# Optimization experiments

Measured on AMD Instinct MI355X. Metric: run time of the kernel, lower is better.

Reference implementation:

```python
import jax, jax.numpy as jnp
import numpy as np

NUM_PARTS = 10
COP_W = 10.0
COP_K = 100.0
RES = 0.7874


def setup_inputs() -> dict:
    key = jax.random.key(0)
    k1, k2, k3, k4, k5, k6 = jax.random.split(key, 6)
    B, V, F, NHD = 256, 6890, 13776, 20000
    vertices = jax.random.normal(k1, (B, V, 3), dtype=jnp.float32)
    pressure = jax.random.uniform(k2, (B, 120, 40), dtype=jnp.float32)
    bw = jax.random.uniform(k3, (NHD, 3), dtype=jnp.float32)
    bary_w = bw / bw.sum(axis=1, keepdims=True)  # barycentric weights sum to 1
    faces = jax.random.randint(k4, (F, 3), 0, V, dtype=jnp.int64)
    face_sample = jax.random.randint(k5, (NHD,), 0, F, dtype=jnp.int64)
    face_part = jax.random.randint(k6, (F,), 0, NUM_PARTS, dtype=jnp.int64)
    return {"vertices": vertices, "pressure": pressure, "bary_w": bary_w,
            "faces": faces, "face_sample": face_sample, "face_part": face_part}


def cal_cop(pressure, resolution=RES):
    B, Y, X = pressure.shape
    x_coords = jnp.arange(X, dtype=pressure.dtype)
    y_coords = jnp.arange(Y, dtype=pressure.dtype)
    total = pressure.sum(axis=(1, 2))
    total = jnp.where(total == 0, jnp.asarray(1e-8, pressure.dtype), total)
    x_ws = (pressure * x_coords).sum(axis=(1, 2))
    y_ws = (pressure * y_coords[:, None]).sum(axis=(1, 2))
    x_c = x_ws / total
    y_c = y_ws / total
    cop_x = 0.01 * (x_c - 18.0) / resolution
    cop_y = 0.01 * (86.0 - y_c) / resolution
    cop_xy = jnp.stack([cop_x, cop_y, jnp.zeros_like(cop_x)], axis=1)
    cop_sensor_xy = jnp.stack([x_c, y_c], axis=1)
    return cop_xy, cop_sensor_xy


def reference(vertices, pressure, bary_w, faces, face_sample, face_part):
    # ---- per-part volume: signed tetrahedron volume per face, segment-summed per part
    tri = vertices[:, faces]                       # [B, F, 3, 3]
    v0, v1, v2 = tri[:, :, 0], tri[:, :, 1], tri[:, :, 2]
    tet = jnp.einsum('bfi,bfi->bf', v0, jnp.cross(v1, v2)) / 6.0   # [B, F]
    per_part_volume = jax.vmap(
        lambda t: jax.ops.segment_sum(t, face_part, num_segments=NUM_PARTS)
    )(tet)                                          # [B, P]

    # ---- HD mesh: barycentric sampling of 20000 points from faces
    fv = faces[face_sample]                         # [NHD, 3]
    vertices_hd = jnp.einsum('bnkc,nk->bnc', vertices[:, fv], bary_w)  # [B, NHD, 3]

    # ---- vertex-id -> part-volume mapping (one-hot sparse matmul == gather)
    vol_per_vert = per_part_volume[:, face_part[face_sample]]          # [B, NHD]

    com = (vertices_hd * vol_per_vert[..., None]).sum(axis=1) / \
          vol_per_vert.sum(axis=1, keepdims=True)                      # [B, 3]
    com_xy = jnp.stack([com[:, 0], com[:, 1], jnp.zeros_like(com[:, 0])], axis=1)
    com_mat = jnp.stack([com[:, 0] * 48.0, (59.0 / 33.0 - com[:, 1]) * 33.0], axis=1)

    cop_xy, _cop_mat = cal_cop(pressure)

    eps = 1e-6
    vh = vertices_hd[:, :, 1]                       # height above ground plane
    inside = (vh < 0.0).astype(vh.dtype)
    pw = inside * (1.0 - COP_K * vh) + (1.0 - inside) * jnp.exp(-COP_W * vh)
    cop = (vertices_hd * pw[..., None]).sum(axis=1) / (pw.sum(axis=1, keepdims=True) + eps)
    cop_mat_ipman = jnp.stack([cop[:, 0] + 18.0 / 78.74,
                               86.0 / 78.74 - cop[:, 1]], axis=1) * 100.0 * 0.7874

    stability_loss = jnp.linalg.norm(com_xy - cop_xy, axis=1).mean()
    return stability_loss, com_mat, cop_mat_ipman
```

## Files before the change

kernel.cpp:

```cpp
#include <hip/hip_runtime.h>
#include <math.h>

#define NB 256
#define NV 6890
#define NF 13776
#define NHD 20000
#define NPARTS 10
#define PY 120
#define PX 40
#define THREADS 1024
#define NWAVES (THREADS / 64)

#define WS_DIST_OFF  0
#define WS_TABF_OFF  1024
#define WS_TABS_OFF  (WS_TABF_OFF + NF * 16)
#define WS_TABW_OFF  (WS_TABS_OFF + NHD * 16)
#define WS_NEEDED    (WS_TABW_OFF + NHD * 16)

__device__ __forceinline__ float wred(float v) {
#pragma unroll
    for (int off = 32; off; off >>= 1) v += __shfl_down(v, off, 64);
    return v;
}

__global__ __launch_bounds__(256) void build_face_tab(const int* __restrict__ faces,
                                                      const int* __restrict__ face_part,
                                                      int4* __restrict__ tabF) {
    const int f = blockIdx.x * 256 + threadIdx.x;
    if (f < NF)
        tabF[f] = make_int4(faces[3 * f + 0], faces[3 * f + 1], faces[3 * f + 2], face_part[f]);
}

__global__ __launch_bounds__(256) void build_samp_tab(const int* __restrict__ faces,
                                                      const int* __restrict__ face_sample,
                                                      const int* __restrict__ face_part,
                                                      const float* __restrict__ bary_w,
                                                      int4* __restrict__ tabS,
                                                      float4* __restrict__ tabW) {
    const int n = blockIdx.x * 256 + threadIdx.x;
    if (n < NHD) {
        const int fs = face_sample[n];
        tabS[n] = make_int4(faces[3 * fs + 0], faces[3 * fs + 1], faces[3 * fs + 2], face_part[fs]);
        tabW[n] = make_float4(bary_w[3 * n + 0], bary_w[3 * n + 1], bary_w[3 * n + 2], 0.0f);
    }
}

template <bool TAB>
__global__ __launch_bounds__(THREADS, 4) void stab_main(
    const float* __restrict__ vertices,
    const float* __restrict__ pressure,
    const float* __restrict__ bary_w,
    const int*   __restrict__ faces,
    const int*   __restrict__ face_sample,
    const int*   __restrict__ face_part,
    const int4*  __restrict__ tabF,
    const int4*  __restrict__ tabS,
    const float4* __restrict__ tabW,
    float* __restrict__ out,
    float* __restrict__ dist)
{
    const int b    = blockIdx.x;
    const int tid  = threadIdx.x;
    const int wave = tid >> 6;
    const int lane = tid & 63;

    __shared__ float2 svxy[NV];
    __shared__ float  svz[NV];
    __shared__ float  red[NWAVES][12];
    __shared__ float  ppv[NPARTS];

    const float* vb = vertices + (size_t)b * (NV * 3);
    for (int v = tid; v < NV; v += THREADS) {
        const float x = vb[3 * v + 0];
        const float y = vb[3 * v + 1];
        const float z = vb[3 * v + 2];
        svxy[v] = make_float2(x, y);
        svz[v]  = z;
    }
    __syncthreads();

    float pv[NPARTS];
#pragma unroll
    for (int p = 0; p < NPARTS; ++p) pv[p] = 0.0f;

    for (int f = tid; f < NF; f += THREADS) {
        int i0, i1, i2, part;
        if constexpr (TAB) {
            const int4 q = tabF[f];
            i0 = q.x; i1 = q.y; i2 = q.z; part = q.w;
        } else {
            i0 = faces[3 * f + 0]; i1 = faces[3 * f + 1]; i2 = faces[3 * f + 2];
            part = face_part[f];
        }
        const float2 a = svxy[i0]; const float az = svz[i0];
        const float2 bb = svxy[i1]; const float bz = svz[i1];
        const float2 cc = svxy[i2]; const float cz = svz[i2];
        const float crx = bb.y * cz - bz * cc.y;
        const float cry = bz * cc.x - bb.x * cz;
        const float crz = bb.x * cc.y - bb.y * cc.x;
        const float tet = (a.x * crx + a.y * cry + az * crz) * (1.0f / 6.0f);
#pragma unroll
        for (int p = 0; p < NPARTS; ++p) pv[p] += (part == p) ? tet : 0.0f;
    }
#pragma unroll
    for (int p = 0; p < NPARTS; ++p) {
        const float r = wred(pv[p]);
        if (lane == 0) red[wave][p] = r;
    }
    __syncthreads();
    if (tid < NPARTS) {
        float s = 0.0f;
#pragma unroll
        for (int w = 0; w < NWAVES; ++w) s += red[w][tid];
        ppv[tid] = s;
    }
    __syncthreads();

    float cnx = 0.f, cny = 0.f, cd = 0.f;
    float pnx = 0.f, pny = 0.f, pd = 0.f;
    for (int n = tid; n < NHD; n += THREADS) {
        int i0, i1, i2, part;
        float w0, w1, w2;
        if constexpr (TAB) {
            const int4 q = tabS[n];
            const float4 w = tabW[n];
            i0 = q.x; i1 = q.y; i2 = q.z; part = q.w;
            w0 = w.x; w1 = w.y; w2 = w.z;
        } else {
            const int fs = face_sample[n];
            i0 = faces[3 * fs + 0]; i1 = faces[3 * fs + 1]; i2 = faces[3 * fs + 2];
            part = face_part[fs];
            w0 = bary_w[3 * n + 0]; w1 = bary_w[3 * n + 1]; w2 = bary_w[3 * n + 2];
        }
        const float2 p0 = svxy[i0];
        const float2 p1 = svxy[i1];
        const float2 p2 = svxy[i2];
        const float hx = w0 * p0.x + w1 * p1.x + w2 * p2.x;
        const float hy = w0 * p0.y + w1 * p1.y + w2 * p2.y;
        const float vol = ppv[part];
        cnx += hx * vol; cny += hy * vol; cd += vol;
        const float pw = (hy < 0.0f) ? (1.0f - 100.0f * hy) : __expf(-10.0f * hy);
        pnx += hx * pw; pny += hy * pw; pd += pw;
    }

    float pt = 0.f, pxs = 0.f, pys = 0.f;
    const float* pb = pressure + (size_t)b * (PY * PX);
    for (int i = tid; i < PY * PX; i += THREADS) {
        const float p  = pb[i];
        const float xi = (float)(i % PX);
        const float yi = (float)(i / PX);
        pt  += p;
        pxs += p * xi;
        pys += p * yi;
    }

    float vals[9] = {cnx, cny, cd, pnx, pny, pd, pt, pxs, pys};
#pragma unroll
    for (int k = 0; k < 9; ++k) {
        const float r = wred(vals[k]);
        if (lane == 0) red[wave][k] = r;
    }
    __syncthreads();

    if (tid == 0) {
        float s[9];
#pragma unroll
        for (int k = 0; k < 9; ++k) {
            float acc = 0.0f;
#pragma unroll
            for (int w = 0; w < NWAVES; ++w) acc += red[w][k];
            s[k] = acc;
        }
        const float comx  = s[0] / s[2];
        const float comy  = s[1] / s[2];
        const float copx  = s[3] / (s[5] + 1e-6f);
        const float copy_ = s[4] / (s[5] + 1e-6f);

        out[1 + 2 * b + 0] = comx * 48.0f;
        out[1 + 2 * b + 1] = (59.0f / 33.0f - comy) * 33.0f;
        out[1 + 2 * NB + 2 * b + 0] = (copx + 18.0f / 78.74f) * (100.0f * 0.7874f);
        out[1 + 2 * NB + 2 * b + 1] = (86.0f / 78.74f - copy_) * (100.0f * 0.7874f);

        const float total = (s[6] == 0.0f) ? 1e-8f : s[6];
        const float xc = s[7] / total;
        const float yc = s[8] / total;
        const float pcopx = 0.01f * (xc - 18.0f) / 0.7874f;
        const float pcopy = 0.01f * (86.0f - yc) / 0.7874f;

        const float dx = comx - pcopx;
        const float dy = comy - pcopy;
        dist[b] = sqrtf(dx * dx + dy * dy);
    }
}

__global__ __launch_bounds__(256) void stab_reduce(const float* __restrict__ dist,
                                                   float* __restrict__ out) {
    const int tid = threadIdx.x;
    float v = dist[tid];
    v = wred(v);
    __shared__ float red[4];
    if ((tid & 63) == 0) red[tid >> 6] = v;
    __syncthreads();
    if (tid == 0) out[0] = (red[0] + red[1] + red[2] + red[3]) * (1.0f / 256.0f);
}

extern "C" void kernel_launch(void* const* d_in, const int* in_sizes, int n_in,
                              void* d_out, int out_size, void* d_ws, size_t ws_size,
                              hipStream_t stream) {
    const float* vertices    = (const float*)d_in[0];
    const float* pressure    = (const float*)d_in[1];
    const float* bary_w      = (const float*)d_in[2];
    const int*   faces       = (const int*)d_in[3];
    const int*   face_sample = (const int*)d_in[4];
    const int*   face_part   = (const int*)d_in[5];
    float* out = (float*)d_out;
    char*  ws  = (char*)d_ws;

    float* dist = (float*)(ws + WS_DIST_OFF);

    if (ws_size >= (size_t)WS_NEEDED) {
        int4*   tabF = (int4*)(ws + WS_TABF_OFF);
        int4*   tabS = (int4*)(ws + WS_TABS_OFF);
        float4* tabW = (float4*)(ws + WS_TABW_OFF);
        build_face_tab<<<(NF + 255) / 256, 256, 0, stream>>>(faces, face_part, tabF);
        build_samp_tab<<<(NHD + 255) / 256, 256, 0, stream>>>(faces, face_sample, face_part,
                                                              bary_w, tabS, tabW);
        stab_main<true><<<NB, THREADS, 0, stream>>>(vertices, pressure, bary_w, faces,
                                                    face_sample, face_part, tabF, tabS, tabW,
                                                    out, dist);
    } else {
        stab_main<false><<<NB, THREADS, 0, stream>>>(vertices, pressure, bary_w, faces,
                                                     face_sample, face_part, nullptr, nullptr,
                                                     nullptr, out, dist);
    }
    stab_reduce<<<1, 256, 0, stream>>>(dist, out);
}
```

Before: 38.30 us.

## Merge table-build kernels, split vertex LDS into SoA, unroll gather loops by four

Merges the two index-table build kernels into one launch, which removes one kernel launch. Shared-memory vertex storage moves from float2+float to three separate float arrays. The face-volume and HD-sample loops in the table path are unrolled by four with clamped indices and masking, so more independent loads and LDS gathers are in flight per thread. The cost is higher register pressure at 1024 threads per block and extra LDS load instructions from the SoA split.

```diff
diff --git a/kernel.cpp b/kernel.cpp
--- a/kernel.cpp
+++ b/kernel.cpp
@@ -23,26 +23,31 @@
     return v;
 }
 
-__global__ __launch_bounds__(256) void build_face_tab(const int* __restrict__ faces,
-                                                      const int* __restrict__ face_part,
-                                                      int4* __restrict__ tabF) {
-    const int f = blockIdx.x * 256 + threadIdx.x;
-    if (f < NF)
-        tabF[f] = make_int4(faces[3 * f + 0], faces[3 * f + 1], faces[3 * f + 2], face_part[f]);
-}
-
-__global__ __launch_bounds__(256) void build_samp_tab(const int* __restrict__ faces,
-                                                      const int* __restrict__ face_sample,
-                                                      const int* __restrict__ face_part,
-                                                      const float* __restrict__ bary_w,
-                                                      int4* __restrict__ tabS,
-                                                      float4* __restrict__ tabW) {
-    const int n = blockIdx.x * 256 + threadIdx.x;
-    if (n < NHD) {
-        const int fs = face_sample[n];
-        tabS[n] = make_int4(faces[3 * fs + 0], faces[3 * fs + 1], faces[3 * fs + 2], face_part[fs]);
-        tabW[n] = make_float4(bary_w[3 * n + 0], bary_w[3 * n + 1], bary_w[3 * n + 2], 0.0f);
-    }
+__global__ __launch_bounds__(256) void build_tabs(const int* __restrict__ faces,
+                                                  const int* __restrict__ face_part,
+                                                  const int* __restrict__ face_sample,
+                                                  const float* __restrict__ bary_w,
+                                                  int4* __restrict__ tabF,
+                                                  int4* __restrict__ tabS,
+                                                  float4* __restrict__ tabW) {
+    const int i = blockIdx.x * 256 + threadIdx.x;
+    if (i < NF)
+        tabF[i] = make_int4(faces[3 * i + 0], faces[3 * i + 1], faces[3 * i + 2], face_part[i]);
+    if (i < NHD) {
+        const int fs = face_sample[i];
+        tabS[i] = make_int4(faces[3 * fs + 0], faces[3 * fs + 1], faces[3 * fs + 2], face_part[fs]);
+        tabW[i] = make_float4(bary_w[3 * i + 0], bary_w[3 * i + 1], bary_w[3 * i + 2], 0.0f);
+    }
+}
+
+__device__ __forceinline__ float tet_of(const float* __restrict__ svx,
+                                        const float* __restrict__ svy,
+                                        const float* __restrict__ svz, int4 q) {
+    const float ax = svx[q.x], bx = svx[q.y], cx = svx[q.z];
+    const float ay = svy[q.x], by = svy[q.y], cy = svy[q.z];
+    const float az = svz[q.x], bz = svz[q.y], cz = svz[q.z];
+    return (ax * (by * cz - bz * cy) + ay * (bz * cx - bx * cz) + az * (bx * cy - by * cx)) *
+           (1.0f / 6.0f);
 }
 
 template <bool TAB>
@@ -64,18 +69,17 @@
     const int wave = tid >> 6;
     const int lane = tid & 63;
 
-    __shared__ float2 svxy[NV];
-    __shared__ float  svz[NV];
-    __shared__ float  red[NWAVES][12];
-    __shared__ float  ppv[NPARTS];
+    __shared__ float svx[NV];
+    __shared__ float svy[NV];
+    __shared__ float svz[NV];
+    __shared__ float red[NWAVES][12];
+    __shared__ float ppv[NPARTS];
 
     const float* vb = vertices + (size_t)b * (NV * 3);
     for (int v = tid; v < NV; v += THREADS) {
-        const float x = vb[3 * v + 0];
-        const float y = vb[3 * v + 1];
-        const float z = vb[3 * v + 2];
-        svxy[v] = make_float2(x, y);
-        svz[v]  = z;
+        svx[v] = vb[3 * v + 0];
+        svy[v] = vb[3 * v + 1];
+        svz[v] = vb[3 * v + 2];
     }
     __syncthreads();
 
@@ -83,24 +87,37 @@
 #pragma unroll
     for (int p = 0; p < NPARTS; ++p) pv[p] = 0.0f;
 
-    for (int f = tid; f < NF; f += THREADS) {
-        int i0, i1, i2, part;
-        if constexpr (TAB) {
-            const int4 q = tabF[f];
-            i0 = q.x; i1 = q.y; i2 = q.z; part = q.w;
-        } else {
-            i0 = faces[3 * f + 0]; i1 = faces[3 * f + 1]; i2 = faces[3 * f + 2];
-            part = face_part[f];
-        }
-        const float2 a = svxy[i0]; const float az = svz[i0];
-        const float2 bb = svxy[i1]; const float bz = svz[i1];
-        const float2 cc = svxy[i2]; const float cz = svz[i2];
-        const float crx = bb.y * cz - bz * cc.y;
-        const float cry = bz * cc.x - bb.x * cz;
-        const float crz = bb.x * cc.y - bb.y * cc.x;
-        const float tet = (a.x * crx + a.y * cry + az * crz) * (1.0f / 6.0f);
-#pragma unroll
-        for (int p = 0; p < NPARTS; ++p) pv[p] += (part == p) ? tet : 0.0f;
+    if constexpr (TAB) {
+        for (int f0 = tid; f0 < NF; f0 += 4 * THREADS) {
+            const int f1 = f0 + THREADS, f2 = f0 + 2 * THREADS, f3 = f0 + 3 * THREADS;
+            const int g1 = min(f1, NF - 1), g2 = min(f2, NF - 1), g3 = min(f3, NF - 1);
+            const int4 q0 = tabF[f0];
+            const int4 q1 = tabF[g1];
+            const int4 q2 = tabF[g2];
+            const int4 q3 = tabF[g3];
+            const float m1 = (f1 < NF) ? 1.0f : 0.0f;
+            const float m2 = (f2 < NF) ? 1.0f : 0.0f;
+            const float m3 = (f3 < NF) ? 1.0f : 0.0f;
+            const float t0 = tet_of(svx, svy, svz, q0);
+            const float t1 = tet_of(svx, svy, svz, q1) * m1;
+            const float t2 = tet_of(svx, svy, svz, q2) * m2;
+            const float t3 = tet_of(svx, svy, svz, q3) * m3;
+#pragma unroll
+            for (int p = 0; p < NPARTS; ++p) {
+                pv[p] += (q0.w == p) ? t0 : 0.0f;
+                pv[p] += (q1.w == p) ? t1 : 0.0f;
+                pv[p] += (q2.w == p) ? t2 : 0.0f;
+                pv[p] += (q3.w == p) ? t3 : 0.0f;
+            }
+        }
+    } else {
+        for (int f = tid; f < NF; f += THREADS) {
+            const int4 q = make_int4(faces[3 * f + 0], faces[3 * f + 1], faces[3 * f + 2],
+                                     face_part[f]);
+            const float t = tet_of(svx, svy, svz, q);
+#pragma unroll
+            for (int p = 0; p < NPARTS; ++p) pv[p] += (q.w == p) ? t : 0.0f;
+        }
     }
 #pragma unroll
     for (int p = 0; p < NPARTS; ++p) {
@@ -118,29 +135,61 @@
 
     float cnx = 0.f, cny = 0.f, cd = 0.f;
     float pnx = 0.f, pny = 0.f, pd = 0.f;
-    for (int n = tid; n < NHD; n += THREADS) {
-        int i0, i1, i2, part;
-        float w0, w1, w2;
-        if constexpr (TAB) {
-            const int4 q = tabS[n];
-            const float4 w = tabW[n];
-            i0 = q.x; i1 = q.y; i2 = q.z; part = q.w;
-            w0 = w.x; w1 = w.y; w2 = w.z;
-        } else {
+
+    if constexpr (TAB) {
+        for (int n0 = tid; n0 < NHD; n0 += 4 * THREADS) {
+            const int n1 = n0 + THREADS, n2 = n0 + 2 * THREADS, n3 = n0 + 3 * THREADS;
+            const int h1 = min(n1, NHD - 1), h2 = min(n2, NHD - 1), h3 = min(n3, NHD - 1);
+            const int4 q0 = tabS[n0];
+            const int4 q1 = tabS[h1];
+            const int4 q2 = tabS[h2];
+            const int4 q3 = tabS[h3];
+            const float4 w0 = tabW[n0];
+            const float4 w1 = tabW[h1];
+            const float4 w2 = tabW[h2];
+            const float4 w3 = tabW[h3];
+            const float m1 = (n1 < NHD) ? 1.0f : 0.0f;
+            const float m2 = (n2 < NHD) ? 1.0f : 0.0f;
+            const float m3 = (n3 < NHD) ? 1.0f : 0.0f;
+
+            const float hx0 = w0.x * svx[q0.x] + w0.y * svx[q0.y] + w0.z * svx[q0.z];
+            const float hy0 = w0.x * svy[q0.x] + w0.y * svy[q0.y] + w0.z * svy[q0.z];
+            const float hx1 = w1.x * svx[q1.x] + w1.y * svx[q1.y] + w1.z * svx[q1.z];
+            const float hy1 = w1.x * svy[q1.x] + w1.y * svy[q1.y] + w1.z * svy[q1.z];
+            const float hx2 = w2.x * svx[q2.x] + w2.y * svx[q2.y] + w2.z * svx[q2.z];
+            const float hy2 = w2.x * svy[q2.x] + w2.y * svy[q2.y] + w2.z * svy[q2.z];
+            const float hx3 = w3.x * svx[q3.x] + w3.y * svx[q3.y] + w3.z * svx[q3.z];
+            const float hy3 = w3.x * svy[q3.x] + w3.y * svy[q3.y] + w3.z * svy[q3.z];
+
+            const float vol0 = ppv[q0.w];
+            const float vol1 = ppv[q1.w] * m1;
+            const float vol2 = ppv[q2.w] * m2;
+            const float vol3 = ppv[q3.w] * m3;
+
+            const float pw0 = ((hy0 < 0.0f) ? (1.0f - 100.0f * hy0) : __expf(-10.0f * hy0));
+            const float pw1 = ((hy1 < 0.0f) ? (1.0f - 100.0f * hy1) : __expf(-10.0f * hy1)) * m1;
+            const float pw2 = ((hy2 < 0.0f) ? (1.0f - 100.0f * hy2) : __expf(-10.0f * hy2)) * m2;
+            const float pw3 = ((hy3 < 0.0f) ? (1.0f - 100.0f * hy3) : __expf(-10.0f * hy3)) * m3;
+
+            cnx += hx0 * vol0 + hx1 * vol1 + hx2 * vol2 + hx3 * vol3;
+            cny += hy0 * vol0 + hy1 * vol1 + hy2 * vol2 + hy3 * vol3;
+            cd  += vol0 + vol1 + vol2 + vol3;
+            pnx += hx0 * pw0 + hx1 * pw1 + hx2 * pw2 + hx3 * pw3;
+            pny += hy0 * pw0 + hy1 * pw1 + hy2 * pw2 + hy3 * pw3;
+            pd  += pw0 + pw1 + pw2 + pw3;
+        }
+    } else {
+        for (int n = tid; n < NHD; n += THREADS) {
             const int fs = face_sample[n];
-            i0 = faces[3 * fs + 0]; i1 = faces[3 * fs + 1]; i2 = faces[3 * fs + 2];
-            part = face_part[fs];
-            w0 = bary_w[3 * n + 0]; w1 = bary_w[3 * n + 1]; w2 = bary_w[3 * n + 2];
-        }
-        const float2 p0 = svxy[i0];
-        const float2 p1 = svxy[i1];
-        const float2 p2 = svxy[i2];
-        const float hx = w0 * p0.x + w1 * p1.x + w2 * p2.x;
-        const float hy = w0 * p0.y + w1 * p1.y + w2 * p2.y;
-        const float vol = ppv[part];
-        cnx += hx * vol; cny += hy * vol; cd += vol;
-        const float pw = (hy < 0.0f) ? (1.0f - 100.0f * hy) : __expf(-10.0f * hy);
-        pnx += hx * pw; pny += hy * pw; pd += pw;
+            const int i0 = faces[3 * fs + 0], i1 = faces[3 * fs + 1], i2 = faces[3 * fs + 2];
+            const float w0 = bary_w[3 * n + 0], w1 = bary_w[3 * n + 1], w2 = bary_w[3 * n + 2];
+            const float hx = w0 * svx[i0] + w1 * svx[i1] + w2 * svx[i2];
+            const float hy = w0 * svy[i0] + w1 * svy[i1] + w2 * svy[i2];
+            const float vol = ppv[face_part[fs]];
+            cnx += hx * vol; cny += hy * vol; cd += vol;
+            const float pw = (hy < 0.0f) ? (1.0f - 100.0f * hy) : __expf(-10.0f * hy);
+            pnx += hx * pw; pny += hy * pw; pd += pw;
+        }
     }
 
     float pt = 0.f, pxs = 0.f, pys = 0.f;
@@ -222,9 +271,8 @@
         int4*   tabF = (int4*)(ws + WS_TABF_OFF);
         int4*   tabS = (int4*)(ws + WS_TABS_OFF);
         float4* tabW = (float4*)(ws + WS_TABW_OFF);
-        build_face_tab<<<(NF + 255) / 256, 256, 0, stream>>>(faces, face_part, tabF);
-        build_samp_tab<<<(NHD + 255) / 256, 256, 0, stream>>>(faces, face_sample, face_part,
-                                                              bary_w, tabS, tabW);
+        build_tabs<<<(NHD + 255) / 256, 256, 0, stream>>>(faces, face_part, face_sample,
+                                                          bary_w, tabF, tabS, tabW);
         stab_main<true><<<NB, THREADS, 0, stream>>>(vertices, pressure, bary_w, faces,
                                                     face_sample, face_part, tabF, tabS, tabW,
                                                     out, dist);
```

Result: faster. 37.23 us (-2.8%).
